# Performance work log

Hardware: AMD Instinct MI355X
Metric: run time of the kernel (lower is better)

The kernel has to match this reference:

```python
import jax, jax.numpy as jnp
import numpy as np

Na, Nb, G, D = 200000, 300000, 10000, 256
EPS_GATE = 1e-6
EPS_BN = 1e-5


def setup_inputs() -> dict:
    key = jax.random.key(0)
    ks = jax.random.split(key, 10)
    h = jax.random.normal(ks[0], (Na, D), jnp.float32)
    e = jax.random.normal(ks[1], (Nb, D), jnp.float32)
    u = jax.random.normal(ks[2], (G, D), jnp.float32)
    snorm_n = jax.random.uniform(ks[3], (Na, 1), jnp.float32)
    snorm_e = jax.random.uniform(ks[4], (Nb, 1), jnp.float32)
    # 9 linear layers A..I stacked: W[i] is [out,in] like nn.Linear.weight
    W = jax.random.normal(ks[5], (9, D, D), jnp.float32) / np.sqrt(D)
    b = jax.random.normal(ks[6], (9, D), jnp.float32) * 0.01
    bn_gamma = jnp.ones((3, D), jnp.float32)
    bn_beta = jnp.zeros((3, D), jnp.float32)
    bond_atoms = jax.random.randint(ks[7], (Nb, 2), 0, Na, dtype=jnp.int32)
    atom2graph = jax.random.randint(ks[8], (Na,), 0, G, dtype=jnp.int32)
    bond2graph = jax.random.randint(ks[9], (Nb,), 0, G, dtype=jnp.int32)
    return {"h": h, "e": e, "u": u, "snorm_n": snorm_n, "snorm_e": snorm_e,
            "W": W, "b": b, "bn_gamma": bn_gamma, "bn_beta": bn_beta,
            "bond_atoms": bond_atoms, "atom2graph": atom2graph,
            "bond2graph": bond2graph}


def reference(h, e, u, snorm_n, snorm_e, W, b, bn_gamma, bn_beta,
              bond_atoms, atom2graph, bond2graph):
    lin = lambda x, i: x @ W[i].T + b[i]
    seg = lambda d, ids, n: jax.ops.segment_sum(d, ids, num_segments=n)

    Ah, Be, Cu = lin(h, 0), lin(e, 1), lin(u, 2)
    Dh, Eh, Fu = lin(h, 3), lin(h, 4), lin(u, 5)
    Gh, He, Iu = lin(h, 6), lin(e, 7), lin(u, 8)

    i0, i1 = bond_atoms[:, 0], bond_atoms[:, 1]
    # bond update: sum of Ah over its 2 atoms + self-loop Be + graph's Cu
    e_new = Ah[i0] + Ah[i1] + Be + Cu[bond2graph]

    # gated b2a aggregation: each endpoint receives sigma(e)*Eh[other endpoint]
    sigma = jax.nn.sigmoid(e_new)  # [Nb, D]
    num = seg(sigma * Eh[i1], i0, Na) + seg(sigma * Eh[i0], i1, Na)
    den = seg(sigma, i0, Na) + seg(sigma, i1, Na)
    h_new = Dh + num / (den + EPS_GATE) + Fu[atom2graph]

    # global update: mean over atoms of Gh + mean over bonds of He + self Iu
    ones_a = jnp.ones((Na, 1), h.dtype)
    ones_b = jnp.ones((Nb, 1), e.dtype)
    cnt_a = jnp.maximum(seg(ones_a, atom2graph, G), 1.0)
    cnt_b = jnp.maximum(seg(ones_b, bond2graph, G), 1.0)
    u_new = seg(Gh, atom2graph, G) / cnt_a + seg(He, bond2graph, G) / cnt_b + Iu

    # graph norm (atoms and bonds only, as in the torch code)
    h_new = h_new * snorm_n
    e_new = e_new * snorm_e

    def bn(x, g, beta):
        m = x.mean(axis=0)
        v = x.var(axis=0)  # biased var, matching BN training normalization
        return g * (x - m) * jax.lax.rsqrt(v + EPS_BN) + beta

    h_out = jax.nn.elu(bn(h_new, bn_gamma[0], bn_beta[0]))
    e_out = jax.nn.elu(bn(e_new, bn_gamma[1], bn_beta[1]))
    u_out = jax.nn.elu(bn(u_new, bn_gamma[2], bn_beta[2]))
    # residual=False (default), dropout=0 -> identity
    return h_out, e_out, u_out
```

## Files before the change

kernel.cpp:

```cpp
#include <hip/hip_runtime.h>
#include <stdint.h>

#define NA 200000
#define NB 300000
#define NG 10000
#define DD 256
#define EPS_GATE 1e-6f
#define EPS_BN 1e-5f

typedef short bf16x8 __attribute__((ext_vector_type(8)));
typedef float f32x4 __attribute__((ext_vector_type(4)));

__device__ __forceinline__ unsigned short f2bf(float f){
  union { float f; uint32_t u; } v; v.f = f;
  uint32_t uu = v.u;
  uint32_t r = (uu + 0x7FFFu + ((uu >> 16) & 1u)) >> 16;
  return (unsigned short)r;
}
__device__ __forceinline__ float bf2f(unsigned short s){
  union { uint32_t u; float f; } v; v.u = ((uint32_t)s) << 16; return v.f;
}

__device__ __forceinline__ void gload_lds16(const unsigned short* g, unsigned short* l){
  __builtin_amdgcn_global_load_lds(
      (const __attribute__((address_space(1))) unsigned int*)g,
      (__attribute__((address_space(3))) unsigned int*)l, 16, 0, 0);
}

__global__ void k_zero(int4* p, size_t n16){
  for (size_t i = blockIdx.x*(size_t)blockDim.x + threadIdx.x; i < n16;
       i += (size_t)gridDim.x*blockDim.x)
    p[i] = make_int4(0,0,0,0);
}

__global__ void k_wconv(const float* __restrict__ W, unsigned short* __restrict__ Wbf, int n4){
  for (int i = blockIdx.x*blockDim.x + threadIdx.x; i < n4; i += gridDim.x*blockDim.x){
    float4 v = ((const float4*)W)[i];
    ushort4 o; o.x = f2bf(v.x); o.y = f2bf(v.y); o.z = f2bf(v.z); o.w = f2bf(v.w);
    ((ushort4*)Wbf)[i] = o;
  }
}

__global__ __launch_bounds__(512, 4) void k_gemm8(
    const float* __restrict__ x, int Nrows,
    const unsigned short* __restrict__ Wbf,
    const float* __restrict__ bias,
    unsigned short* __restrict__ Y,
    int j0, int j1, int j2, int j3, int nW)
{
  __shared__ unsigned short As[96*256];
  __shared__ unsigned short Bs[2*256*32];
  const int tid  = threadIdx.x;
  const int wave = tid >> 6, lane = tid & 63;
  const int l15  = lane & 15, kq = lane >> 4;
  const int wr   = wave >> 2, wc = wave & 3;
  const int rowBase = blockIdx.x * 96;

  #pragma unroll
  for (int i = 0; i < 6; ++i){
    int idx = i*512 + tid;
    int r = idx >> 5, g = idx & 31;
    f32x4 v0 = {0.f,0.f,0.f,0.f}, v1 = {0.f,0.f,0.f,0.f};
    if (rowBase + r < Nrows){
      const float* p = x + (size_t)(rowBase + r)*DD + g*8;
      v0 = *(const f32x4*)p; v1 = *(const f32x4*)(p + 4);
    }
    uint32_t d[4];
    const uint32_t* a  = (const uint32_t*)&v0;
    const uint32_t* b2 = (const uint32_t*)&v1;
    d[0] = __builtin_amdgcn_perm(a[1],  a[0],  0x07060302u);
    d[1] = __builtin_amdgcn_perm(a[3],  a[2],  0x07060302u);
    d[2] = __builtin_amdgcn_perm(b2[1], b2[0], 0x07060302u);
    d[3] = __builtin_amdgcn_perm(b2[3], b2[2], 0x07060302u);
    int gs = g ^ ((r & 15) << 1);
    *(int4*)(As + r*256 + gs*8) = *(int4*)d;
  }

  const int sB = kq ^ ((l15 >> 1) & 3);

  auto pick = [&](int jj)->int { return (jj==0) ? j0 : (jj==1) ? j1 : (jj==2) ? j2 : j3; };

  auto stageB = [&](int j, int ks, int buf){
    const unsigned short* Wj = Wbf + (size_t)j*DD*DD + ks*32;
    unsigned short* dst = Bs + (size_t)buf*(256*32);
    #pragma unroll
    for (int i = 0; i < 2; ++i){
      int idx  = i*512 + tid;
      int row  = idx >> 2;
      int slot = idx & 3;
      int srcg = slot ^ ((row >> 1) & 3);
      gload_lds16(Wj + (size_t)row*DD + srcg*8,
                  dst + ((size_t)i*512 + wave*64)*8);
    }
  };

  stageB(pick(0), 0, 0);
  __syncthreads();

  for (int jj = 0; jj < nW; ++jj){
    const int j = pick(jj);
    f32x4 acc[3][4];
    #pragma unroll
    for (int m=0;m<3;m++)
      #pragma unroll
      for (int n=0;n<4;n++)
        acc[m][n] = (f32x4){0.f,0.f,0.f,0.f};

    #pragma unroll
    for (int ks = 0; ks < 8; ++ks){
      if (ks < 7){
        stageB(j, ks+1, (ks+1)&1);
        asm volatile("s_waitcnt vmcnt(2)" ::: "memory");
      } else {
        asm volatile("s_waitcnt vmcnt(0)" ::: "memory");
      }
      __builtin_amdgcn_s_barrier();

      const unsigned short* Bb = Bs + (size_t)(ks&1)*(256*32);
      bf16x8 afr[3], bfr[4];
      #pragma unroll
      for (int m=0;m<3;m++){
        int row = wr*48 + 16*m + l15;
        int gs = (ks*4 + kq) ^ (l15 << 1);
        afr[m] = *(const bf16x8*)(As + row*256 + gs*8);
      }
      #pragma unroll
      for (int n=0;n<4;n++){
        int row = wc*64 + 16*n + l15;
        bfr[n] = *(const bf16x8*)(Bb + row*32 + sB*8);
      }
      #pragma unroll
      for (int m=0;m<3;m++)
        #pragma unroll
        for (int n=0;n<4;n++)
          acc[m][n] = __builtin_amdgcn_mfma_f32_16x16x32_bf16(afr[m], bfr[n], acc[m][n], 0,0,0);

      __builtin_amdgcn_s_barrier();
    }

    const float* bj = bias + (size_t)j*DD;
    unsigned short* Yj = Y + (size_t)jj*Nrows*DD;
    #pragma unroll
    for (int m=0;m<3;m++){
      int row0 = rowBase + wr*48 + 16*m + 4*kq;
      #pragma unroll
      for (int n=0;n<4;n++){
        int col = wc*64 + 16*n + l15;
        float bv = bj[col];
        #pragma unroll
        for (int r=0;r<4;r++){
          int row = row0 + r;
          if (row < Nrows) Yj[(size_t)row*DD + col] = f2bf(acc[m][n][r] + bv);
        }
      }
    }

    if (jj+1 < nW) stageB(pick(jj+1), 0, 0);
  }
}

__global__ void k_hist(const int* __restrict__ ba, const int* __restrict__ b2g,
                       const int* __restrict__ a2g,
                       int* deg, int* cntb, int* cnta){
  int stride = gridDim.x*blockDim.x;
  for (int i = blockIdx.x*blockDim.x + threadIdx.x; i < NB; i += stride){
    atomicAdd(&deg[ba[2*i]],   1);
    atomicAdd(&deg[ba[2*i+1]], 1);
    atomicAdd(&cntb[b2g[i]],   1);
  }
  for (int i = blockIdx.x*blockDim.x + threadIdx.x; i < NA; i += stride)
    atomicAdd(&cnta[a2g[i]], 1);
}

__global__ void k_scan_partials(const int* __restrict__ in, int n, int* __restrict__ part){
  __shared__ int sd[256];
  int base = blockIdx.x*2048;
  int s = 0;
  #pragma unroll
  for (int i=0;i<8;i++){
    int idx = base + threadIdx.x*8 + i;
    if (idx < n) s += in[idx];
  }
  sd[threadIdx.x] = s;
  __syncthreads();
  for (int off=128; off>0; off>>=1){
    if (threadIdx.x < off) sd[threadIdx.x] += sd[threadIdx.x+off];
    __syncthreads();
  }
  if (threadIdx.x==0) part[blockIdx.x] = sd[0];
}
__global__ void k_scan_small(int* part, int nb){
  if (threadIdx.x==0 && blockIdx.x==0){
    int run = 0;
    for (int i=0;i<nb;i++){ int v = part[i]; part[i] = run; run += v; }
    part[nb] = run;
  }
}
__global__ void k_scan_final(const int* __restrict__ in, int n,
                             const int* __restrict__ part, int* __restrict__ outp){
  __shared__ int sd[256];
  int base = blockIdx.x*2048;
  int loc[8];
  int s = 0;
  #pragma unroll
  for (int i=0;i<8;i++){
    int idx = base + threadIdx.x*8 + i;
    int v = (idx < n) ? in[idx] : 0;
    loc[i] = s; s += v;
  }
  sd[threadIdx.x] = s;
  __syncthreads();
  int mine = s;
  for (int off=1; off<256; off<<=1){
    int add = (threadIdx.x >= off) ? sd[threadIdx.x - off] : 0;
    __syncthreads();
    sd[threadIdx.x] += add;
    __syncthreads();
  }
  int b0 = part[blockIdx.x] + sd[threadIdx.x] - mine;
  #pragma unroll
  for (int i=0;i<8;i++){
    int idx = base + threadIdx.x*8 + i;
    if (idx < n) outp[idx] = b0 + loc[i];
  }
  if (blockIdx.x==0 && threadIdx.x==0) outp[n] = part[gridDim.x];
}

__global__ void k_scatter_atoms(const int* __restrict__ a2g, const int* __restrict__ goffa,
                                int* cura, int* alist){
  for (int i = blockIdx.x*blockDim.x + threadIdx.x; i < NA; i += gridDim.x*blockDim.x){
    int g = a2g[i];
    int p = atomicAdd(&cura[g], 1);
    alist[goffa[g] + p] = i;
  }
}
__global__ void k_scatter_bonds(const int* __restrict__ ba, const int* __restrict__ b2g,
                                const int* __restrict__ goffb, int* curb, int* blist,
                                const int* __restrict__ aoff, int* cur_atom,
                                int* incb, int* inco){
  for (int i = blockIdx.x*blockDim.x + threadIdx.x; i < NB; i += gridDim.x*blockDim.x){
    int g = b2g[i];
    int p = atomicAdd(&curb[g], 1);
    blist[goffb[g] + p] = i;
    int i0 = ba[2*i], i1 = ba[2*i+1];
    int q0 = atomicAdd(&cur_atom[i0], 1);
    incb[aoff[i0]+q0] = i; inco[aoff[i0]+q0] = i1;
    int q1 = atomicAdd(&cur_atom[i1], 1);
    incb[aoff[i1]+q1] = i; inco[aoff[i1]+q1] = i0;
  }
}

__global__ __launch_bounds__(256) void k_bond(
    const unsigned short* __restrict__ Ah, unsigned short* __restrict__ Be,
    const unsigned short* __restrict__ Cu,
    const int* __restrict__ ba, const int* __restrict__ b2g,
    const float* __restrict__ sne,
    unsigned short* __restrict__ Sg,
    float* esum, float* esumsq)
{
  const int wave = threadIdx.x >> 6, lane = threadIdx.x & 63;
  float s1[4] = {0,0,0,0}, s2[4] = {0,0,0,0};
  const int wstride = gridDim.x*4;

  for (int bond = blockIdx.x*4 + wave; bond < NB; bond += 2*wstride){
    const int bondB = bond + wstride;
    const bool hasB = bondB < NB;
    const int bB = hasB ? bondB : bond;

    int i0  = ba[2*bond], i1  = ba[2*bond+1];
    int i0B = ba[2*bB],   i1B = ba[2*bB+1];
    int g   = b2g[bond],  gB  = b2g[bB];
    float sn = sne[bond], snB = sne[bB];

    ushort4 a0  = *(const ushort4*)(Ah + (size_t)i0 *DD + lane*4);
    ushort4 a1  = *(const ushort4*)(Ah + (size_t)i1 *DD + lane*4);
    ushort4 be  = *(const ushort4*)(Be + (size_t)bond*DD + lane*4);
    ushort4 cu  = *(const ushort4*)(Cu + (size_t)g  *DD + lane*4);
    ushort4 a0B = *(const ushort4*)(Ah + (size_t)i0B*DD + lane*4);
    ushort4 a1B = *(const ushort4*)(Ah + (size_t)i1B*DD + lane*4);
    ushort4 beB = *(const ushort4*)(Be + (size_t)bB *DD + lane*4);
    ushort4 cuB = *(const ushort4*)(Cu + (size_t)gB *DD + lane*4);

    {
      float e0 = bf2f(a0.x)+bf2f(a1.x)+bf2f(be.x)+bf2f(cu.x);
      float e1 = bf2f(a0.y)+bf2f(a1.y)+bf2f(be.y)+bf2f(cu.y);
      float e2 = bf2f(a0.z)+bf2f(a1.z)+bf2f(be.z)+bf2f(cu.z);
      float e3 = bf2f(a0.w)+bf2f(a1.w)+bf2f(be.w)+bf2f(cu.w);
      ushort4 sg;
      sg.x = f2bf(1.f/(1.f+__expf(-e0)));
      sg.y = f2bf(1.f/(1.f+__expf(-e1)));
      sg.z = f2bf(1.f/(1.f+__expf(-e2)));
      sg.w = f2bf(1.f/(1.f+__expf(-e3)));
      *(ushort4*)(Sg + (size_t)bond*DD + lane*4) = sg;
      float p0 = e0*sn, p1 = e1*sn, p2 = e2*sn, p3 = e3*sn;
      ushort4 eb; eb.x = f2bf(p0); eb.y = f2bf(p1); eb.z = f2bf(p2); eb.w = f2bf(p3);
      *(ushort4*)(Be + (size_t)bond*DD + lane*4) = eb;
      s1[0]+=p0; s2[0]+=p0*p0;  s1[1]+=p1; s2[1]+=p1*p1;
      s1[2]+=p2; s2[2]+=p2*p2;  s1[3]+=p3; s2[3]+=p3*p3;
    }
    if (hasB){
      float e0 = bf2f(a0B.x)+bf2f(a1B.x)+bf2f(beB.x)+bf2f(cuB.x);
      float e1 = bf2f(a0B.y)+bf2f(a1B.y)+bf2f(beB.y)+bf2f(cuB.y);
      float e2 = bf2f(a0B.z)+bf2f(a1B.z)+bf2f(beB.z)+bf2f(cuB.z);
      float e3 = bf2f(a0B.w)+bf2f(a1B.w)+bf2f(beB.w)+bf2f(cuB.w);
      ushort4 sg;
      sg.x = f2bf(1.f/(1.f+__expf(-e0)));
      sg.y = f2bf(1.f/(1.f+__expf(-e1)));
      sg.z = f2bf(1.f/(1.f+__expf(-e2)));
      sg.w = f2bf(1.f/(1.f+__expf(-e3)));
      *(ushort4*)(Sg + (size_t)bB*DD + lane*4) = sg;
      float p0 = e0*snB, p1 = e1*snB, p2 = e2*snB, p3 = e3*snB;
      ushort4 eb; eb.x = f2bf(p0); eb.y = f2bf(p1); eb.z = f2bf(p2); eb.w = f2bf(p3);
      *(ushort4*)(Be + (size_t)bB*DD + lane*4) = eb;
      s1[0]+=p0; s2[0]+=p0*p0;  s1[1]+=p1; s2[1]+=p1*p1;
      s1[2]+=p2; s2[2]+=p2*p2;  s1[3]+=p3; s2[3]+=p3*p3;
    }
  }
  __shared__ float red[4*DD];
  #pragma unroll
  for (int c=0;c<4;c++) red[wave*DD + lane*4 + c] = s1[c];
  __syncthreads();
  if (threadIdx.x < DD){
    float t = red[threadIdx.x] + red[DD+threadIdx.x] + red[2*DD+threadIdx.x] + red[3*DD+threadIdx.x];
    atomicAdd(&esum[threadIdx.x], t);
  }
  __syncthreads();
  #pragma unroll
  for (int c=0;c<4;c++) red[wave*DD + lane*4 + c] = s2[c];
  __syncthreads();
  if (threadIdx.x < DD){
    float t = red[threadIdx.x] + red[DD+threadIdx.x] + red[2*DD+threadIdx.x] + red[3*DD+threadIdx.x];
    atomicAdd(&esumsq[threadIdx.x], t);
  }
}

__global__ __launch_bounds__(256) void k_atom(
    unsigned short* __restrict__ Dh,
    const unsigned short* __restrict__ Eh,
    const unsigned short* __restrict__ Fu, const unsigned short* __restrict__ Sg,
    const int* __restrict__ aoff, const int* __restrict__ incb, const int* __restrict__ inco,
    const int* __restrict__ a2g, const float* __restrict__ snn,
    float* hsum, float* hsumsq)
{
  const int wave = threadIdx.x >> 6, lane = threadIdx.x & 63;
  float s1[4] = {0,0,0,0}, s2[4] = {0,0,0,0};
  const int wstride = gridDim.x*4;
  for (int a = blockIdx.x*4 + wave; a < NA; a += wstride){
    int j0 = aoff[a], j1 = aoff[a+1];
    int g = a2g[a]; float sn = snn[a];
    ushort4 dh = *(const ushort4*)(Dh + (size_t)a*DD + lane*4);
    ushort4 fu = *(const ushort4*)(Fu + (size_t)g*DD + lane*4);

    float num[4] = {0,0,0,0}, den[4] = {0,0,0,0};
    int j = j0;
    for (; j + 2 <= j1; j += 2){
      int b0 = incb[j],   o0 = inco[j];
      int b1 = incb[j+1], o1 = inco[j+1];
      ushort4 sg0 = *(const ushort4*)(Sg + (size_t)b0*DD + lane*4);
      ushort4 eo0 = *(const ushort4*)(Eh + (size_t)o0*DD + lane*4);
      ushort4 sg1 = *(const ushort4*)(Sg + (size_t)b1*DD + lane*4);
      ushort4 eo1 = *(const ushort4*)(Eh + (size_t)o1*DD + lane*4);
      float g0 = bf2f(sg0.x), g1 = bf2f(sg0.y), g2 = bf2f(sg0.z), g3 = bf2f(sg0.w);
      num[0] += g0*bf2f(eo0.x); num[1] += g1*bf2f(eo0.y);
      num[2] += g2*bf2f(eo0.z); num[3] += g3*bf2f(eo0.w);
      den[0] += g0; den[1] += g1; den[2] += g2; den[3] += g3;
      float h0 = bf2f(sg1.x), h1 = bf2f(sg1.y), h2 = bf2f(sg1.z), h3 = bf2f(sg1.w);
      num[0] += h0*bf2f(eo1.x); num[1] += h1*bf2f(eo1.y);
      num[2] += h2*bf2f(eo1.z); num[3] += h3*bf2f(eo1.w);
      den[0] += h0; den[1] += h1; den[2] += h2; den[3] += h3;
    }
    if (j < j1){
      int b0 = incb[j], o0 = inco[j];
      ushort4 sg0 = *(const ushort4*)(Sg + (size_t)b0*DD + lane*4);
      ushort4 eo0 = *(const ushort4*)(Eh + (size_t)o0*DD + lane*4);
      float g0 = bf2f(sg0.x), g1 = bf2f(sg0.y), g2 = bf2f(sg0.z), g3 = bf2f(sg0.w);
      num[0] += g0*bf2f(eo0.x); num[1] += g1*bf2f(eo0.y);
      num[2] += g2*bf2f(eo0.z); num[3] += g3*bf2f(eo0.w);
      den[0] += g0; den[1] += g1; den[2] += g2; den[3] += g3;
    }

    float h0 = (bf2f(dh.x) + num[0]/(den[0]+EPS_GATE) + bf2f(fu.x))*sn;
    float h1 = (bf2f(dh.y) + num[1]/(den[1]+EPS_GATE) + bf2f(fu.y))*sn;
    float h2 = (bf2f(dh.z) + num[2]/(den[2]+EPS_GATE) + bf2f(fu.z))*sn;
    float h3 = (bf2f(dh.w) + num[3]/(den[3]+EPS_GATE) + bf2f(fu.w))*sn;
    ushort4 hb; hb.x = f2bf(h0); hb.y = f2bf(h1); hb.z = f2bf(h2); hb.w = f2bf(h3);
    *(ushort4*)(Dh + (size_t)a*DD + lane*4) = hb;
    s1[0]+=h0; s2[0]+=h0*h0;  s1[1]+=h1; s2[1]+=h1*h1;
    s1[2]+=h2; s2[2]+=h2*h2;  s1[3]+=h3; s2[3]+=h3*h3;
  }
  __shared__ float red[4*DD];
  #pragma unroll
  for (int c=0;c<4;c++) red[wave*DD + lane*4 + c] = s1[c];
  __syncthreads();
  if (threadIdx.x < DD){
    float t = red[threadIdx.x] + red[DD+threadIdx.x] + red[2*DD+threadIdx.x] + red[3*DD+threadIdx.x];
    atomicAdd(&hsum[threadIdx.x], t);
  }
  __syncthreads();
  #pragma unroll
  for (int c=0;c<4;c++) red[wave*DD + lane*4 + c] = s2[c];
  __syncthreads();
  if (threadIdx.x < DD){
    float t = red[threadIdx.x] + red[DD+threadIdx.x] + red[2*DD+threadIdx.x] + red[3*DD+threadIdx.x];
    atomicAdd(&hsumsq[threadIdx.x], t);
  }
}

__global__ __launch_bounds__(256) void k_graph(
    const unsigned short* __restrict__ Gh, const unsigned short* __restrict__ He,
    const unsigned short* __restrict__ Iu,
    const int* __restrict__ goffa, const int* __restrict__ alist,
    const int* __restrict__ goffb, const int* __restrict__ blist,
    float* __restrict__ u_pre)
{
  int g = blockIdx.x, t = threadIdx.x;
  int a0 = goffa[g], a1 = goffa[g+1];
  float sA = 0.f;
  {
    int i = a0;
    for (; i + 4 <= a1; i += 4){
      int r0 = alist[i], r1 = alist[i+1], r2 = alist[i+2], r3 = alist[i+3];
      float v0 = bf2f(Gh[(size_t)r0*DD + t]);
      float v1 = bf2f(Gh[(size_t)r1*DD + t]);
      float v2 = bf2f(Gh[(size_t)r2*DD + t]);
      float v3 = bf2f(Gh[(size_t)r3*DD + t]);
      sA += (v0 + v1) + (v2 + v3);
    }
    for (; i < a1; ++i) sA += bf2f(Gh[(size_t)alist[i]*DD + t]);
  }
  int b0 = goffb[g], b1 = goffb[g+1];
  float sB = 0.f;
  {
    int i = b0;
    for (; i + 4 <= b1; i += 4){
      int r0 = blist[i], r1 = blist[i+1], r2 = blist[i+2], r3 = blist[i+3];
      float v0 = bf2f(He[(size_t)r0*DD + t]);
      float v1 = bf2f(He[(size_t)r1*DD + t]);
      float v2 = bf2f(He[(size_t)r2*DD + t]);
      float v3 = bf2f(He[(size_t)r3*DD + t]);
      sB += (v0 + v1) + (v2 + v3);
    }
    for (; i < b1; ++i) sB += bf2f(He[(size_t)blist[i]*DD + t]);
  }
  float cA = (float)max(a1 - a0, 1);
  float cB = (float)max(b1 - b0, 1);
  u_pre[(size_t)g*DD + t] = sA/cA + sB/cB + bf2f(Iu[(size_t)g*DD + t]);
}

__global__ void k_ustats(const float* __restrict__ u_pre, float* usum, float* usumsq){
  int t = threadIdx.x;
  float s = 0.f, s2 = 0.f;
  for (int g = blockIdx.x; g < NG; g += gridDim.x){
    float v = u_pre[(size_t)g*DD + t];
    s += v; s2 += v*v;
  }
  atomicAdd(&usum[t], s);
  atomicAdd(&usumsq[t], s2);
}

__global__ void k_bnfin(const float* __restrict__ sums, const float* __restrict__ sumsq,
                        float* __restrict__ mr){
  int o = blockIdx.x, t = threadIdx.x;
  float n = (o==0) ? (float)NA : (o==1) ? (float)NB : (float)NG;
  float m = sums[o*DD+t]/n;
  float v = sumsq[o*DD+t]/n - m*m;
  mr[o*2*DD + t]      = m;
  mr[o*2*DD + DD + t] = rsqrtf(fmaxf(v, 0.f) + EPS_BN);
}

__global__ __launch_bounds__(256) void k_norm_bf(
    const unsigned short* __restrict__ src, float* __restrict__ dst, size_t nrows,
    const float* __restrict__ mr, const float* __restrict__ gamma,
    const float* __restrict__ beta)
{
  __shared__ float sm[DD], sr[DD], sg[DD], sb[DD];
  int t = threadIdx.x;
  sm[t] = mr[t]; sr[t] = mr[DD+t]; sg[t] = gamma[t]; sb[t] = beta[t];
  __syncthreads();
  size_t total = nrows*(DD/4);
  for (size_t i = blockIdx.x*(size_t)blockDim.x + t; i < total;
       i += (size_t)gridDim.x*blockDim.x){
    int c = ((int)(i & 63))*4;
    ushort4 s = ((const ushort4*)src)[i];
    float z0 = (bf2f(s.x) - sm[c+0])*sr[c+0]*sg[c+0] + sb[c+0];
    float z1 = (bf2f(s.y) - sm[c+1])*sr[c+1]*sg[c+1] + sb[c+1];
    float z2 = (bf2f(s.z) - sm[c+2])*sr[c+2]*sg[c+2] + sb[c+2];
    float z3 = (bf2f(s.w) - sm[c+3])*sr[c+3]*sg[c+3] + sb[c+3];
    float4 v;
    v.x = z0 > 0.f ? z0 : expm1f(z0);
    v.y = z1 > 0.f ? z1 : expm1f(z1);
    v.z = z2 > 0.f ? z2 : expm1f(z2);
    v.w = z3 > 0.f ? z3 : expm1f(z3);
    ((float4*)dst)[i] = v;
  }
}

__global__ __launch_bounds__(256) void k_norm_f32(
    float* __restrict__ buf, size_t nrows,
    const float* __restrict__ mr, const float* __restrict__ gamma,
    const float* __restrict__ beta)
{
  __shared__ float sm[DD], sr[DD], sg[DD], sb[DD];
  int t = threadIdx.x;
  sm[t] = mr[t]; sr[t] = mr[DD+t]; sg[t] = gamma[t]; sb[t] = beta[t];
  __syncthreads();
  size_t total = nrows*(DD/4);
  for (size_t i = blockIdx.x*(size_t)blockDim.x + t; i < total;
       i += (size_t)gridDim.x*blockDim.x){
    int c = ((int)(i & 63))*4;
    float4 v = ((float4*)buf)[i];
    float z0 = (v.x - sm[c+0])*sr[c+0]*sg[c+0] + sb[c+0];
    float z1 = (v.y - sm[c+1])*sr[c+1]*sg[c+1] + sb[c+1];
    float z2 = (v.z - sm[c+2])*sr[c+2]*sg[c+2] + sb[c+2];
    float z3 = (v.w - sm[c+3])*sr[c+3]*sg[c+3] + sb[c+3];
    v.x = z0 > 0.f ? z0 : expm1f(z0);
    v.y = z1 > 0.f ? z1 : expm1f(z1);
    v.z = z2 > 0.f ? z2 : expm1f(z2);
    v.w = z3 > 0.f ? z3 : expm1f(z3);
    ((float4*)buf)[i] = v;
  }
}

extern "C" void kernel_launch(void* const* d_in, const int* in_sizes, int n_in,
                              void* d_out, int out_size, void* d_ws, size_t ws_size,
                              hipStream_t stream)
{
  (void)in_sizes; (void)n_in; (void)out_size;
  const float* h   = (const float*)d_in[0];
  const float* e   = (const float*)d_in[1];
  const float* u   = (const float*)d_in[2];
  const float* snn = (const float*)d_in[3];
  const float* sne = (const float*)d_in[4];
  const float* W   = (const float*)d_in[5];
  const float* b   = (const float*)d_in[6];
  const float* gamma = (const float*)d_in[7];
  const float* beta  = (const float*)d_in[8];
  const int* ba  = (const int*)d_in[9];
  const int* a2g = (const int*)d_in[10];
  const int* b2g = (const int*)d_in[11];

  float* outp  = (float*)d_out;
  float* h_out = outp;
  float* e_out = outp + (size_t)NA*DD;
  float* u_pre = outp + (size_t)(NA+NB)*DD;

  char* ws = (char*)d_ws;
  size_t off = 0;
  auto alloc = [&](size_t bytes)->char* {
    char* p = ws + off;
    off += (bytes + 255) & ~(size_t)255;
    return p;
  };
  unsigned short* Wbf = (unsigned short*)alloc((size_t)9*DD*DD*2);
  unsigned short* Yh  = (unsigned short*)alloc((size_t)4*NA*DD*2);
  unsigned short* Ye  = (unsigned short*)alloc((size_t)2*NB*DD*2);
  unsigned short* Yu  = (unsigned short*)alloc((size_t)3*NG*DD*2);
  unsigned short* Sg  = (unsigned short*)alloc((size_t)NB*DD*2);
  int* aoff  = (int*)alloc((size_t)(NA+1)*4);
  int* goffa = (int*)alloc((size_t)(NG+1)*4);
  int* goffb = (int*)alloc((size_t)(NG+1)*4);
  int* alist = (int*)alloc((size_t)NA*4);
  int* blist = (int*)alloc((size_t)NB*4);
  int* incb  = (int*)alloc((size_t)2*NB*4);
  int* inco  = (int*)alloc((size_t)2*NB*4);
  int* part  = (int*)alloc(1024);
  float* mr  = (float*)alloc((size_t)3*2*DD*4);
  char* zz   = ws + off;
  int* deg      = (int*)alloc((size_t)NA*4);
  int* cur_atom = (int*)alloc((size_t)NA*4);
  int* cnta  = (int*)alloc((size_t)NG*4);
  int* cntb  = (int*)alloc((size_t)NG*4);
  int* cura  = (int*)alloc((size_t)NG*4);
  int* curb  = (int*)alloc((size_t)NG*4);
  float* sums  = (float*)alloc((size_t)3*DD*4);
  float* sumsq = (float*)alloc((size_t)3*DD*4);
  size_t zbytes = (size_t)((ws + off) - zz);

  if (ws_size < off) return;

  unsigned short* Ah = Yh;
  unsigned short* Dh = Yh + (size_t)1*NA*DD;
  unsigned short* Eh = Yh + (size_t)2*NA*DD;
  unsigned short* Gh = Yh + (size_t)3*NA*DD;
  unsigned short* Be = Ye;
  unsigned short* He = Ye + (size_t)NB*DD;
  unsigned short* Cu = Yu;
  unsigned short* Fu = Yu + (size_t)1*NG*DD;
  unsigned short* Iu = Yu + (size_t)2*NG*DD;

  k_zero<<<256, 256, 0, stream>>>((int4*)zz, zbytes/16);
  k_wconv<<<288, 256, 0, stream>>>(W, Wbf, 9*DD*DD/4);

  k_gemm8<<<(NA+95)/96, 512, 0, stream>>>(h, NA, Wbf, b, Yh, 0,3,4,6, 4);
  k_gemm8<<<(NB+95)/96, 512, 0, stream>>>(e, NB, Wbf, b, Ye, 1,7,0,0, 2);
  k_gemm8<<<(NG+95)/96, 512, 0, stream>>>(u, NG, Wbf, b, Yu, 2,5,8,0, 3);

  k_hist<<<1024, 256, 0, stream>>>(ba, b2g, a2g, deg, cntb, cnta);

  k_scan_partials<<<98, 256, 0, stream>>>(deg, NA, part);
  k_scan_small<<<1, 64, 0, stream>>>(part, 98);
  k_scan_final<<<98, 256, 0, stream>>>(deg, NA, part, aoff);
  k_scan_partials<<<5, 256, 0, stream>>>(cnta, NG, part);
  k_scan_small<<<1, 64, 0, stream>>>(part, 5);
  k_scan_final<<<5, 256, 0, stream>>>(cnta, NG, part, goffa);
  k_scan_partials<<<5, 256, 0, stream>>>(cntb, NG, part);
  k_scan_small<<<1, 64, 0, stream>>>(part, 5);
  k_scan_final<<<5, 256, 0, stream>>>(cntb, NG, part, goffb);

  k_scatter_atoms<<<512, 256, 0, stream>>>(a2g, goffa, cura, alist);
  k_scatter_bonds<<<512, 256, 0, stream>>>(ba, b2g, goffb, curb, blist,
                                           aoff, cur_atom, incb, inco);

  k_bond<<<2048, 256, 0, stream>>>(Ah, Be, Cu, ba, b2g, sne, Sg,
                                   sums + DD, sumsq + DD);
  k_atom<<<2048, 256, 0, stream>>>(Dh, Eh, Fu, Sg, aoff, incb, inco, a2g, snn,
                                   sums + 0, sumsq + 0);
  k_graph<<<NG, 256, 0, stream>>>(Gh, He, Iu, goffa, alist, goffb, blist, u_pre);
  k_ustats<<<40, 256, 0, stream>>>(u_pre, sums + 2*DD, sumsq + 2*DD);

  k_bnfin<<<3, 256, 0, stream>>>(sums, sumsq, mr);

  k_norm_bf<<<2048, 256, 0, stream>>>(Dh, h_out, (size_t)NA, mr + 0,    gamma + 0,    beta + 0);
  k_norm_bf<<<2048, 256, 0, stream>>>(Be, e_out, (size_t)NB, mr + 2*DD, gamma + DD,   beta + DD);
  k_norm_f32<<<64,  256, 0, stream>>>(u_pre, (size_t)NG, mr + 4*DD,     gamma + 2*DD, beta + 2*DD);
}
```

Before: 1.347 ms.

## Double GEMM row tile to 192 with 1024-thread blocks; unroll atom gather by four

```diff
diff --git a/kernel.cpp b/kernel.cpp
--- a/kernel.cpp
+++ b/kernel.cpp
@@ -41,24 +41,24 @@
   }
 }
 
-__global__ __launch_bounds__(512, 4) void k_gemm8(
+__global__ __launch_bounds__(1024, 4) void k_gemm9(
     const float* __restrict__ x, int Nrows,
     const unsigned short* __restrict__ Wbf,
     const float* __restrict__ bias,
     unsigned short* __restrict__ Y,
     int j0, int j1, int j2, int j3, int nW)
 {
-  __shared__ unsigned short As[96*256];
+  __shared__ unsigned short As[192*256];
   __shared__ unsigned short Bs[2*256*32];
   const int tid  = threadIdx.x;
   const int wave = tid >> 6, lane = tid & 63;
   const int l15  = lane & 15, kq = lane >> 4;
   const int wr   = wave >> 2, wc = wave & 3;
-  const int rowBase = blockIdx.x * 96;
+  const int rowBase = blockIdx.x * 192;
 
   #pragma unroll
   for (int i = 0; i < 6; ++i){
-    int idx = i*512 + tid;
+    int idx = i*1024 + tid;
     int r = idx >> 5, g = idx & 31;
     f32x4 v0 = {0.f,0.f,0.f,0.f}, v1 = {0.f,0.f,0.f,0.f};
     if (rowBase + r < Nrows){
@@ -83,15 +83,10 @@
   auto stageB = [&](int j, int ks, int buf){
     const unsigned short* Wj = Wbf + (size_t)j*DD*DD + ks*32;
     unsigned short* dst = Bs + (size_t)buf*(256*32);
-    #pragma unroll
-    for (int i = 0; i < 2; ++i){
-      int idx  = i*512 + tid;
-      int row  = idx >> 2;
-      int slot = idx & 3;
-      int srcg = slot ^ ((row >> 1) & 3);
-      gload_lds16(Wj + (size_t)row*DD + srcg*8,
-                  dst + ((size_t)i*512 + wave*64)*8);
-    }
+    int row  = tid >> 2;
+    int slot = tid & 3;
+    int srcg = slot ^ ((row >> 1) & 3);
+    gload_lds16(Wj + (size_t)row*DD + srcg*8, dst + (size_t)(wave*64)*8);
   };
 
   stageB(pick(0), 0, 0);
@@ -110,7 +105,7 @@
     for (int ks = 0; ks < 8; ++ks){
       if (ks < 7){
         stageB(j, ks+1, (ks+1)&1);
-        asm volatile("s_waitcnt vmcnt(2)" ::: "memory");
+        asm volatile("s_waitcnt vmcnt(1)" ::: "memory");
       } else {
         asm volatile("s_waitcnt vmcnt(0)" ::: "memory");
       }
@@ -352,7 +347,28 @@
     ushort4 fu = *(const ushort4*)(Fu + (size_t)g*DD + lane*4);
 
     float num[4] = {0,0,0,0}, den[4] = {0,0,0,0};
+    auto accum = [&](const ushort4& sgv, const ushort4& eov){
+      float g0 = bf2f(sgv.x), g1 = bf2f(sgv.y), g2 = bf2f(sgv.z), g3 = bf2f(sgv.w);
+      num[0] += g0*bf2f(eov.x); num[1] += g1*bf2f(eov.y);
+      num[2] += g2*bf2f(eov.z); num[3] += g3*bf2f(eov.w);
+      den[0] += g0; den[1] += g1; den[2] += g2; den[3] += g3;
+    };
     int j = j0;
+    for (; j + 4 <= j1; j += 4){
+      int b0 = incb[j],   o0 = inco[j];
+      int b1 = incb[j+1], o1 = inco[j+1];
+      int b2 = incb[j+2], o2 = inco[j+2];
+      int b3 = incb[j+3], o3 = inco[j+3];
+      ushort4 sg0 = *(const ushort4*)(Sg + (size_t)b0*DD + lane*4);
+      ushort4 eo0 = *(const ushort4*)(Eh + (size_t)o0*DD + lane*4);
+      ushort4 sg1 = *(const ushort4*)(Sg + (size_t)b1*DD + lane*4);
+      ushort4 eo1 = *(const ushort4*)(Eh + (size_t)o1*DD + lane*4);
+      ushort4 sg2 = *(const ushort4*)(Sg + (size_t)b2*DD + lane*4);
+      ushort4 eo2 = *(const ushort4*)(Eh + (size_t)o2*DD + lane*4);
+      ushort4 sg3 = *(const ushort4*)(Sg + (size_t)b3*DD + lane*4);
+      ushort4 eo3 = *(const ushort4*)(Eh + (size_t)o3*DD + lane*4);
+      accum(sg0, eo0); accum(sg1, eo1); accum(sg2, eo2); accum(sg3, eo3);
+    }
     for (; j + 2 <= j1; j += 2){
       int b0 = incb[j],   o0 = inco[j];
       int b1 = incb[j+1], o1 = inco[j+1];
@@ -360,23 +376,13 @@
       ushort4 eo0 = *(const ushort4*)(Eh + (size_t)o0*DD + lane*4);
       ushort4 sg1 = *(const ushort4*)(Sg + (size_t)b1*DD + lane*4);
       ushort4 eo1 = *(const ushort4*)(Eh + (size_t)o1*DD + lane*4);
-      float g0 = bf2f(sg0.x), g1 = bf2f(sg0.y), g2 = bf2f(sg0.z), g3 = bf2f(sg0.w);
-      num[0] += g0*bf2f(eo0.x); num[1] += g1*bf2f(eo0.y);
-      num[2] += g2*bf2f(eo0.z); num[3] += g3*bf2f(eo0.w);
-      den[0] += g0; den[1] += g1; den[2] += g2; den[3] += g3;
-      float h0 = bf2f(sg1.x), h1 = bf2f(sg1.y), h2 = bf2f(sg1.z), h3 = bf2f(sg1.w);
-      num[0] += h0*bf2f(eo1.x); num[1] += h1*bf2f(eo1.y);
-      num[2] += h2*bf2f(eo1.z); num[3] += h3*bf2f(eo1.w);
-      den[0] += h0; den[1] += h1; den[2] += h2; den[3] += h3;
+      accum(sg0, eo0); accum(sg1, eo1);
     }
     if (j < j1){
       int b0 = incb[j], o0 = inco[j];
       ushort4 sg0 = *(const ushort4*)(Sg + (size_t)b0*DD + lane*4);
       ushort4 eo0 = *(const ushort4*)(Eh + (size_t)o0*DD + lane*4);
-      float g0 = bf2f(sg0.x), g1 = bf2f(sg0.y), g2 = bf2f(sg0.z), g3 = bf2f(sg0.w);
-      num[0] += g0*bf2f(eo0.x); num[1] += g1*bf2f(eo0.y);
-      num[2] += g2*bf2f(eo0.z); num[3] += g3*bf2f(eo0.w);
-      den[0] += g0; den[1] += g1; den[2] += g2; den[3] += g3;
+      accum(sg0, eo0);
     }
 
     float h0 = (bf2f(dh.x) + num[0]/(den[0]+EPS_GATE) + bf2f(fu.x))*sn;
@@ -591,9 +597,9 @@
   k_zero<<<256, 256, 0, stream>>>((int4*)zz, zbytes/16);
   k_wconv<<<288, 256, 0, stream>>>(W, Wbf, 9*DD*DD/4);
 
-  k_gemm8<<<(NA+95)/96, 512, 0, stream>>>(h, NA, Wbf, b, Yh, 0,3,4,6, 4);
-  k_gemm8<<<(NB+95)/96, 512, 0, stream>>>(e, NB, Wbf, b, Ye, 1,7,0,0, 2);
-  k_gemm8<<<(NG+95)/96, 512, 0, stream>>>(u, NG, Wbf, b, Yu, 2,5,8,0, 3);
+  k_gemm9<<<(NA+191)/192, 1024, 0, stream>>>(h, NA, Wbf, b, Yh, 0,3,4,6, 4);
+  k_gemm9<<<(NB+191)/192, 1024, 0, stream>>>(e, NB, Wbf, b, Ye, 1,7,0,0, 2);
+  k_gemm9<<<(NG+191)/192, 1024, 0, stream>>>(u, NG, Wbf, b, Yu, 2,5,8,0, 3);
 
   k_hist<<<1024, 256, 0, stream>>>(ba, b2g, a2g, deg, cntb, cnta);
 
```

New measurement: 1.387 ms. 3.0% more time.
